# Optimization experiments

Measured on AMD Instinct MI355X. Metric: run time of the kernel, lower is better.

## Reference

```python
import jax, jax.numpy as jnp
import numpy as np

HIDDEN = 128
N_RBF = 20
K = 16
CUTOFF = 5.0


def setup_inputs() -> dict:
    key = jax.random.key(0)
    ks = jax.random.split(key, 12)
    B, N, D = 8, 4096, HIDDEN
    edge_in = 2 * D + N_RBF  # 276
    s = 0.02
    return {
        "h": jax.random.normal(ks[0], (B, N, D), jnp.float32),
        "positions": jax.random.normal(ks[1], (B, N, 3), jnp.float32),
        # edge MLP: Linear(276->128), SiLU, Linear(128->128), SiLU
        "ew1": jax.random.normal(ks[2], (edge_in, D), jnp.float32) * s,
        "eb1": jnp.zeros((D,), jnp.float32),
        "ew2": jax.random.normal(ks[3], (D, D), jnp.float32) * s,
        "eb2": jnp.zeros((D,), jnp.float32),
        # node MLP: Linear(256->128), SiLU, (Dropout=identity in eval), Linear(128->128)
        "nw1": jax.random.normal(ks[4], (2 * D, D), jnp.float32) * s,
        "nb1": jnp.zeros((D,), jnp.float32),
        "nw2": jax.random.normal(ks[5], (D, D), jnp.float32) * s,
        "nb2": jnp.zeros((D,), jnp.float32),
        # LayerNorm
        "gamma": jnp.ones((D,), jnp.float32),
        "beta": jnp.zeros((D,), jnp.float32),
    }


def reference(h, positions, ew1, eb1, ew2, eb2, nw1, nb1, nw2, nb2, gamma, beta):
    B, N, D = h.shape
    k = min(K, N - 1)

    # ---- kNN graph build (dense pairwise, self masked with +inf) ----
    diff = positions[:, :, None, :] - positions[:, None, :, :]      # [B,N,N,3]
    dists = jnp.sqrt(jnp.sum(diff * diff, axis=-1) + 1e-8)          # [B,N,N]
    eye = jnp.eye(N, dtype=bool)
    dists_masked = jnp.where(eye[None], jnp.inf, dists)
    _, edge_idx = jax.lax.top_k(-dists_masked, k)                   # [B,N,k] smallest dists
    edge_dist = jnp.take_along_axis(dists_masked, edge_idx, axis=-1)  # [B,N,k]
    edge_mask = edge_dist < CUTOFF                                  # [B,N,k]

    # ---- RBF distance encoding (non-trainable buffers) ----
    centers = jnp.linspace(0.0, CUTOFF, N_RBF)                      # [n_rbf]
    widths = (CUTOFF / N_RBF) ** (-2)
    rbf = jnp.exp(-widths * (edge_dist[..., None] - centers) ** 2)  # [B,N,k,n_rbf]

    # ---- gather neighbor features ----
    h_j = jax.vmap(lambda hb, ib: hb[ib])(h, edge_idx)              # [B,N,k,D]
    h_i = jnp.broadcast_to(h[:, :, None, :], h_j.shape)             # [B,N,k,D]
    edge_features = jnp.concatenate([h_i, h_j, rbf], axis=-1)       # [B,N,k,2D+n_rbf]

    # ---- edge MLP + mask + scatter-sum aggregate ----
    m = jax.nn.silu(edge_features @ ew1 + eb1)
    m = jax.nn.silu(m @ ew2 + eb2)
    m = m * edge_mask[..., None].astype(m.dtype)
    agg = jnp.sum(m, axis=2)                                        # [B,N,D]

    # ---- node MLP (dropout is identity at eval) + residual + LayerNorm ----
    node_in = jnp.concatenate([h, agg], axis=-1)                    # [B,N,2D]
    update = jax.nn.silu(node_in @ nw1 + nb1) @ nw2 + nb2
    x = h + update
    mu = jnp.mean(x, axis=-1, keepdims=True)
    var = jnp.mean((x - mu) ** 2, axis=-1, keepdims=True)
    return (x - mu) / jnp.sqrt(var + 1e-5) * gamma + beta
```

## Files before the change

### kernel.cpp

```cpp
#include <hip/hip_runtime.h>

#define HID 128
#define NRBF 20
#define KNN 16
#define NNODE 4096
#define NBATCH 8
#define CAP 112

typedef __attribute__((ext_vector_type(8))) short short8;
typedef __attribute__((ext_vector_type(4))) float f32x4;

__device__ __forceinline__ short f2bf(float x) {
  unsigned u = __builtin_bit_cast(unsigned, x);
  u = u + 0x7FFFu + ((u >> 16) & 1u);
  return (short)(u >> 16);
}
__device__ __forceinline__ float silu_f(float x) {
  return x * __builtin_amdgcn_rcpf(1.0f + __expf(-x));
}
__device__ __forceinline__ short8 cv8(const float* p) {
  f32x4 a = *(const f32x4*)p;
  f32x4 b = *(const f32x4*)(p + 4);
  short8 r;
  r[0]=f2bf(a[0]); r[1]=f2bf(a[1]); r[2]=f2bf(a[2]); r[3]=f2bf(a[3]);
  r[4]=f2bf(b[0]); r[5]=f2bf(b[1]); r[6]=f2bf(b[2]); r[7]=f2bf(b[3]);
  return r;
}

__global__ __launch_bounds__(256)
void hcvt_kernel(const float* __restrict__ h, short* __restrict__ hb)
{
  size_t i = ((size_t)blockIdx.x * 256 + threadIdx.x) * 8;
  *(short8*)(hb + i) = cv8(h + i);
}

__global__ __launch_bounds__(512)
void knn_kernel(const float* __restrict__ pos,
                int* __restrict__ eidx, float* __restrict__ edist)
{
  __shared__ float pX[NNODE], pY[NNODE], pZ[NNODE];
  __shared__ float d2b[8][4][CAP];
  __shared__ int   jb[8][4][CAP];
  __shared__ int   cntL[8][4];

  const int tid  = threadIdx.x;
  const int wv   = tid >> 6;
  const int lane = tid & 63;
  const int b    = blockIdx.x >> 7;
  const int grp  = blockIdx.x & 127;

  const float* pb = pos + (size_t)b * NNODE * 3;
  for (int idx = tid; idx < NNODE; idx += 512) {
    pX[idx] = pb[idx*3]; pY[idx] = pb[idx*3+1]; pZ[idx] = pb[idx*3+2];
  }
  __syncthreads();

  const int i0 = grp * 32 + wv * 4;
  float pix[4], piy[4], piz[4];
  #pragma unroll
  for (int n = 0; n < 4; ++n) { pix[n]=pX[i0+n]; piy[n]=pY[i0+n]; piz[n]=pZ[i0+n]; }

  float vmin0[4] = {3.0e38f, 3.0e38f, 3.0e38f, 3.0e38f};
  float vmin1[4] = {3.0e38f, 3.0e38f, 3.0e38f, 3.0e38f};
  #pragma unroll 4
  for (int t = 0; t < 64; t += 2) {
    const int j0 = t*64 + lane, j1 = j0 + 64;
    const float x0 = pX[j0], y0 = pY[j0], z0 = pZ[j0];
    const float x1 = pX[j1], y1 = pY[j1], z1 = pZ[j1];
    #pragma unroll
    for (int n = 0; n < 4; ++n) {
      float dx0 = pix[n]-x0, dy0 = piy[n]-y0, dz0 = piz[n]-z0;
      vmin0[n] = fminf(vmin0[n], fmaf(dz0,dz0, fmaf(dy0,dy0, dx0*dx0)));
      float dx1 = pix[n]-x1, dy1 = piy[n]-y1, dz1 = piz[n]-z1;
      vmin1[n] = fminf(vmin1[n], fmaf(dz1,dz1, fmaf(dy1,dy1, dx1*dx1)));
    }
  }

  float Tp[4];
  #pragma unroll
  for (int n = 0; n < 4; ++n) {
    float v = fminf(vmin0[n], vmin1[n]);
    #pragma unroll
    for (int k = 2; k <= 64; k <<= 1) {
      #pragma unroll
      for (int jj = k >> 1; jj > 0; jj >>= 1) {
        float o = __shfl_xor(v, jj);
        const bool up   = ((lane & k) == 0);
        const bool lowl = ((lane & jj) == 0);
        float mn = fminf(v, o), mx = fmaxf(v, o);
        v = (up == lowl) ? mn : mx;
      }
    }
    float Tf = __shfl(v, 16);
    Tp[n] = Tf * (1.0f + 2.0e-6f) + 1.0e-35f;
  }

  if (lane < 4) cntL[wv][lane] = 0;
  #pragma unroll 2
  for (int t = 0; t < 64; ++t) {
    const int j = t * 64 + lane;
    const float x = pX[j], y = pY[j], z = pZ[j];
    #pragma unroll
    for (int n = 0; n < 4; ++n) {
      float dx = pix[n] - x, dy = piy[n] - y, dz = piz[n] - z;
      float d2 = fmaf(dz, dz, fmaf(dy, dy, dx * dx));
      if ((j != i0 + n) && (d2 <= Tp[n])) {
        int p = atomicAdd(&cntL[wv][n], 1);
        if (p < CAP) jb[wv][n][p] = j;
      }
    }
  }

  #pragma unroll 1
  for (int n = 0; n < 4; ++n) {
    int cnt = cntL[wv][n];
    if (cnt > CAP) cnt = CAP;
    for (int s = lane; s < cnt; s += 64) {
      int j = jb[wv][n][s];
      float dx = __fsub_rn(pix[n], pX[j]);
      float dy = __fsub_rn(piy[n], pY[j]);
      float dz = __fsub_rn(piz[n], pZ[j]);
      d2b[wv][n][s] = __fadd_rn(__fadd_rn(__fmul_rn(dx,dx), __fmul_rn(dy,dy)),
                                __fmul_rn(dz,dz));
    }
    for (int s = lane; s < cnt; s += 64) {
      float dm = d2b[wv][n][s]; int jm = jb[wv][n][s];
      int rank = 0;
      for (int c = 0; c < cnt; ++c) {
        float dc = d2b[wv][n][c]; int jc = jb[wv][n][c];
        if (dc < dm || (dc == dm && jc < jm)) ++rank;
      }
      if (rank < KNN) {
        size_t base = ((size_t)b * NNODE + i0 + n) * KNN;
        eidx[base + rank]  = b * NNODE + jm;
        edist[base + rank] = sqrtf(__fadd_rn(dm, 1e-8f));
      }
    }
  }
}

#define ENPW 16

template<bool HBF>
__global__ __launch_bounds__(512)
void edge_kernel(const float* __restrict__ h, const short* __restrict__ hb,
                 const int* __restrict__ eidx, const float* __restrict__ edist,
                 const float* __restrict__ ew1, const float* __restrict__ eb1,
                 const float* __restrict__ ew2, const float* __restrict__ eb2,
                 float* __restrict__ agg)
{
  __shared__ __attribute__((aligned(16))) short8 F1[9*8*64];
  __shared__ __attribute__((aligned(16))) short8 F2[4*8*64];
  __shared__ __attribute__((aligned(16))) short m1s[8][2048];

  const int tid = threadIdx.x;
  for (int f = tid; f < 9*8*64; f += 512) {
    int kc = f >> 9, rem = f & 511, nf = rem >> 6, ln = rem & 63;
    int kb = kc*32 + (ln >> 4)*8, col = nf*16 + (ln & 15);
    short8 v;
    #pragma unroll
    for (int e = 0; e < 8; ++e) {
      int k = kb + e;
      v[e] = (k < 276) ? f2bf(ew1[k*128 + col]) : (short)0;
    }
    F1[f] = v;
  }
  for (int f = tid; f < 4*8*64; f += 512) {
    int kc = f >> 9, rem = f & 511, nf = rem >> 6, ln = rem & 63;
    int kb = kc*32 + (ln >> 4)*8, col = nf*16 + (ln & 15);
    short8 v;
    #pragma unroll
    for (int e = 0; e < 8; ++e) v[e] = f2bf(ew2[(kb + e)*128 + col]);
    F2[f] = v;
  }
  __syncthreads();

  const int wv = tid >> 6, lane = tid & 63;
  const int lo = lane & 15, hi = lane >> 4;
  short* m1w = &m1s[wv][0];

  float b1v[8], b2v[8];
  #pragma unroll
  for (int nf = 0; nf < 8; ++nf) {
    b1v[nf] = eb1[nf*16 + lo];
    b2v[nf] = eb2[nf*16 + lo];
  }
  int wbase[4], xmask[4], rbase[4];
  #pragma unroll
  for (int q = 0; q < 4; ++q) {
    int row = hi*4 + q;
    wbase[q] = (row << 8) + (lo << 1);
    xmask[q] = (row & 7) << 4;
  }
  #pragma unroll
  for (int kc = 0; kc < 4; ++kc)
    rbase[kc] = ((lo << 8) + ((kc*32 + hi*8) << 1)) ^ ((lo & 7) << 4);

  const f32x4 zero4 = {0.f, 0.f, 0.f, 0.f};
  const int nbase = (blockIdx.x * 8 + wv) * ENPW;

  int   jgA_p = eidx[(size_t)(nbase+0)*KNN + lo] & (NBATCH*NNODE - 1);
  int   jgB_p = eidx[(size_t)(nbase+1)*KNN + lo] & (NBATCH*NNODE - 1);
  float deA_p = edist[(size_t)(nbase+0)*KNN + lo];
  float deB_p = edist[(size_t)(nbase+1)*KNN + lo];

  #pragma unroll 1
  for (int it = 0; it < ENPW/2; ++it) {
    const int nA = nbase + it*2, nB = nA + 1;
    const int jgA = jgA_p, jgB = jgB_p;
    const float deA = deA_p, deB = deB_p;

    short8 aIA[4], aJA[4], aIB[4], aJB[4];
    #pragma unroll
    for (int kc = 0; kc < 4; ++kc) {
      if constexpr (HBF) {
        aIA[kc] = *(const short8*)(hb + (size_t)nA*HID  + kc*32 + hi*8);
        aJA[kc] = *(const short8*)(hb + (size_t)jgA*HID + kc*32 + hi*8);
        aIB[kc] = *(const short8*)(hb + (size_t)nB*HID  + kc*32 + hi*8);
        aJB[kc] = *(const short8*)(hb + (size_t)jgB*HID + kc*32 + hi*8);
      } else {
        aIA[kc] = cv8(h + (size_t)nA*HID  + kc*32 + hi*8);
        aJA[kc] = cv8(h + (size_t)jgA*HID + kc*32 + hi*8);
        aIB[kc] = cv8(h + (size_t)nB*HID  + kc*32 + hi*8);
        aJB[kc] = cv8(h + (size_t)jgB*HID + kc*32 + hi*8);
      }
    }

    if (it < ENPW/2 - 1) {
      jgA_p = eidx[(size_t)(nA+2)*KNN + lo] & (NBATCH*NNODE - 1);
      jgB_p = eidx[(size_t)(nB+2)*KNN + lo] & (NBATCH*NNODE - 1);
      deA_p = edist[(size_t)(nA+2)*KNN + lo];
      deB_p = edist[(size_t)(nB+2)*KNN + lo];
    }

    short8 aRA, aRB;
    #pragma unroll
    for (int e = 0; e < 8; ++e) {
      const int r = hi*8 + e;
      float vA = 0.f, vB = 0.f;
      if (r < NRBF) {
        const float cr = (float)(r * (5.0/19.0));
        float tA = __fsub_rn(deA, cr), tB = __fsub_rn(deB, cr);
        vA = __expf(-16.0f * __fmul_rn(tA, tA));
        vB = __expf(-16.0f * __fmul_rn(tB, tB));
      }
      aRA[e] = f2bf(vA); aRB[e] = f2bf(vB);
    }

    f32x4 acc1A[8], acc1B[8];
    #pragma unroll
    for (int nf = 0; nf < 8; ++nf) { acc1A[nf] = zero4; acc1B[nf] = zero4; }
    __builtin_amdgcn_s_setprio(1);
    #pragma unroll
    for (int kc = 0; kc < 9; ++kc) {
      short8 aA = (kc < 4) ? aIA[kc] : ((kc < 8) ? aJA[kc-4] : aRA);
      short8 aB = (kc < 4) ? aIB[kc] : ((kc < 8) ? aJB[kc-4] : aRB);
      #pragma unroll
      for (int nf = 0; nf < 8; ++nf) {
        short8 bfv = F1[(kc*8 + nf)*64 + lane];
        acc1A[nf] = __builtin_amdgcn_mfma_f32_16x16x32_bf16(aA, bfv, acc1A[nf], 0,0,0);
        acc1B[nf] = __builtin_amdgcn_mfma_f32_16x16x32_bf16(aB, bfv, acc1B[nf], 0,0,0);
      }
    }
    __builtin_amdgcn_s_setprio(0);

    short8 a2A[4], a2B[4];
    #pragma unroll
    for (int nf = 0; nf < 8; ++nf) {
      #pragma unroll
      for (int q = 0; q < 4; ++q) {
        int off = (wbase[q] + (nf << 5)) ^ xmask[q];
        *(short*)((char*)m1w + off) = f2bf(silu_f(acc1A[nf][q] + b1v[nf]));
      }
    }
    #pragma unroll
    for (int kc = 0; kc < 4; ++kc)
      a2A[kc] = *(const short8*)((char*)m1w + rbase[kc]);
    #pragma unroll
    for (int nf = 0; nf < 8; ++nf) {
      #pragma unroll
      for (int q = 0; q < 4; ++q) {
        int off = (wbase[q] + (nf << 5)) ^ xmask[q];
        *(short*)((char*)m1w + off) = f2bf(silu_f(acc1B[nf][q] + b1v[nf]));
      }
    }
    #pragma unroll
    for (int kc = 0; kc < 4; ++kc)
      a2B[kc] = *(const short8*)((char*)m1w + rbase[kc]);

    f32x4 acc2A[8], acc2B[8];
    #pragma unroll
    for (int nf = 0; nf < 8; ++nf) { acc2A[nf] = zero4; acc2B[nf] = zero4; }
    __builtin_amdgcn_s_setprio(1);
    #pragma unroll
    for (int kc = 0; kc < 4; ++kc) {
      #pragma unroll
      for (int nf = 0; nf < 8; ++nf) {
        short8 bfv = F2[(kc*8 + nf)*64 + lane];
        acc2A[nf] = __builtin_amdgcn_mfma_f32_16x16x32_bf16(a2A[kc], bfv, acc2A[nf], 0,0,0);
        acc2B[nf] = __builtin_amdgcn_mfma_f32_16x16x32_bf16(a2B[kc], bfv, acc2B[nf], 0,0,0);
      }
    }
    __builtin_amdgcn_s_setprio(0);

    float dqA[4], dqB[4];
    #pragma unroll
    for (int q = 0; q < 4; ++q) {
      dqA[q] = __shfl(deA, hi*4 + q);
      dqB[q] = __shfl(deB, hi*4 + q);
    }
    #pragma unroll
    for (int nf = 0; nf < 8; ++nf) {
      float sA = 0.f, sB = 0.f;
      #pragma unroll
      for (int q = 0; q < 4; ++q) {
        float mA = silu_f(acc2A[nf][q] + b2v[nf]);
        float mB = silu_f(acc2B[nf][q] + b2v[nf]);
        sA += (dqA[q] < 5.0f) ? mA : 0.f;
        sB += (dqB[q] < 5.0f) ? mB : 0.f;
      }
      sA += __shfl_xor(sA, 16); sA += __shfl_xor(sA, 32);
      sB += __shfl_xor(sB, 16); sB += __shfl_xor(sB, 32);
      if (hi == 0) {
        agg[(size_t)nA*HID + nf*16 + lo] = sA;
        agg[(size_t)nB*HID + nf*16 + lo] = sB;
      }
    }
  }
}

template<bool HBF>
__global__ __launch_bounds__(512)
void node_kernel(const float* __restrict__ h, const short* __restrict__ hb,
                 const float* agg,
                 const float* __restrict__ nw1, const float* __restrict__ nb1,
                 const float* __restrict__ nw2, const float* __restrict__ nb2,
                 const float* __restrict__ gam, const float* __restrict__ bet,
                 float* out)
{
  __shared__ __attribute__((aligned(16))) short8 G1[8*8*64];
  __shared__ __attribute__((aligned(16))) short8 G2[4*8*64];
  __shared__ __attribute__((aligned(16))) short m1s[8][2048];

  const int tid = threadIdx.x;
  for (int f = tid; f < 8*8*64; f += 512) {
    int kc = f >> 9, rem = f & 511, nf = rem >> 6, ln = rem & 63;
    int kb = kc*32 + (ln >> 4)*8, col = nf*16 + (ln & 15);
    short8 v;
    #pragma unroll
    for (int e = 0; e < 8; ++e) v[e] = f2bf(nw1[(kb + e)*128 + col]);
    G1[f] = v;
  }
  for (int f = tid; f < 4*8*64; f += 512) {
    int kc = f >> 9, rem = f & 511, nf = rem >> 6, ln = rem & 63;
    int kb = kc*32 + (ln >> 4)*8, col = nf*16 + (ln & 15);
    short8 v;
    #pragma unroll
    for (int e = 0; e < 8; ++e) v[e] = f2bf(nw2[(kb + e)*128 + col]);
    G2[f] = v;
  }
  __syncthreads();

  const int wv = tid >> 6, lane = tid & 63;
  const int lo = lane & 15, hi = lane >> 4;
  short* m1w = &m1s[wv][0];

  float b1v[8], b2v[8], gv[8], bv[8];
  #pragma unroll
  for (int nf = 0; nf < 8; ++nf) {
    b1v[nf] = nb1[nf*16 + lo];
    b2v[nf] = nb2[nf*16 + lo];
    gv[nf]  = gam[nf*16 + lo];
    bv[nf]  = bet[nf*16 + lo];
  }
  const f32x4 zero4 = {0.f, 0.f, 0.f, 0.f};

  const int row0 = (blockIdx.x * 8 + wv) * 16;

  const float* hrow = h   + (size_t)(row0 + lo) * HID;
  const float* arow = agg + (size_t)(row0 + lo) * HID;
  const short* hbrow = hb + (size_t)(row0 + lo) * HID;

  f32x4 acc1[8];
  #pragma unroll
  for (int nf = 0; nf < 8; ++nf) acc1[nf] = zero4;
  #pragma unroll
  for (int kc = 0; kc < 8; ++kc) {
    short8 a;
    if (kc < 4) {
      if constexpr (HBF) a = *(const short8*)(hbrow + kc*32 + hi*8);
      else               a = cv8(hrow + kc*32 + hi*8);
    } else {
      a = cv8(arow + (kc - 4)*32 + hi*8);
    }
    #pragma unroll
    for (int nf = 0; nf < 8; ++nf) {
      short8 bfv = G1[(kc*8 + nf)*64 + lane];
      acc1[nf] = __builtin_amdgcn_mfma_f32_16x16x32_bf16(a, bfv, acc1[nf], 0,0,0);
    }
  }

  #pragma unroll
  for (int nf = 0; nf < 8; ++nf) {
    #pragma unroll
    for (int q = 0; q < 4; ++q) {
      float s = silu_f(acc1[nf][q] + b1v[nf]);
      int row = hi*4 + q, col = nf*16 + lo;
      int byteoff = ((row << 8) + (col << 1)) ^ ((row & 7) << 4);
      *(short*)((char*)m1w + byteoff) = f2bf(s);
    }
  }

  f32x4 acc2[8];
  #pragma unroll
  for (int nf = 0; nf < 8; ++nf) acc2[nf] = zero4;
  #pragma unroll
  for (int kc = 0; kc < 4; ++kc) {
    int byteA = ((lo << 8) + ((kc*32 + hi*8) << 1)) ^ ((lo & 7) << 4);
    short8 a = *(const short8*)((char*)m1w + byteA);
    #pragma unroll
    for (int nf = 0; nf < 8; ++nf) {
      short8 bfv = G2[(kc*8 + nf)*64 + lane];
      acc2[nf] = __builtin_amdgcn_mfma_f32_16x16x32_bf16(a, bfv, acc2[nf], 0,0,0);
    }
  }

  float xv[4][8];
  #pragma unroll
  for (int nf = 0; nf < 8; ++nf) {
    #pragma unroll
    for (int q = 0; q < 4; ++q) {
      xv[q][nf] = acc2[nf][q] + b2v[nf]
                + h[(size_t)(row0 + hi*4 + q) * HID + nf*16 + lo];
    }
  }

  #pragma unroll
  for (int q = 0; q < 4; ++q) {
    float s = 0.0f;
    #pragma unroll
    for (int nf = 0; nf < 8; ++nf) s += xv[q][nf];
    s += __shfl_xor(s, 1); s += __shfl_xor(s, 2);
    s += __shfl_xor(s, 4); s += __shfl_xor(s, 8);
    float mu = s * 0.0078125f;
    float t = 0.0f;
    #pragma unroll
    for (int nf = 0; nf < 8; ++nf) { float d = xv[q][nf] - mu; t += d * d; }
    t += __shfl_xor(t, 1); t += __shfl_xor(t, 2);
    t += __shfl_xor(t, 4); t += __shfl_xor(t, 8);
    float inv = 1.0f / sqrtf(t * 0.0078125f + 1e-5f);
    #pragma unroll
    for (int nf = 0; nf < 8; ++nf) {
      float y = (xv[q][nf] - mu) * inv * gv[nf] + bv[nf];
      out[(size_t)(row0 + hi*4 + q) * HID + nf*16 + lo] = y;
    }
  }
}

extern "C" void kernel_launch(void* const* d_in, const int* in_sizes, int n_in,
                              void* d_out, int out_size, void* d_ws, size_t ws_size,
                              hipStream_t stream) {
  (void)in_sizes; (void)n_in; (void)out_size;
  const float* h   = (const float*)d_in[0];
  const float* pos = (const float*)d_in[1];
  const float* ew1 = (const float*)d_in[2];
  const float* eb1 = (const float*)d_in[3];
  const float* ew2 = (const float*)d_in[4];
  const float* eb2 = (const float*)d_in[5];
  const float* nw1 = (const float*)d_in[6];
  const float* nb1 = (const float*)d_in[7];
  const float* nw2 = (const float*)d_in[8];
  const float* nb2 = (const float*)d_in[9];
  const float* gam = (const float*)d_in[10];
  const float* bet = (const float*)d_in[11];

  const size_t base_need = (size_t)NBATCH * NNODE * KNN * 8;
  const size_t hbf_need  = base_need + (size_t)NBATCH * NNODE * HID * 2;
  if (ws_size < base_need) return;
  const bool use_hbf = (ws_size >= hbf_need);

  char* wsp = (char*)d_ws;
  int*   eidx  = (int*)wsp;
  float* edist = (float*)(wsp + (size_t)NBATCH * NNODE * KNN * 4);
  short* hb    = (short*)(wsp + base_need);
  float* agg   = (float*)d_out;

  if (use_hbf) {
    hcvt_kernel<<<dim3(2048), dim3(256), 0, stream>>>(h, hb);
  }
  knn_kernel<<<dim3(1024), dim3(512), 0, stream>>>(pos, eidx, edist);
  if (use_hbf) {
    edge_kernel<true ><<<dim3(256), dim3(512), 0, stream>>>(h, hb, eidx, edist,
                                                            ew1, eb1, ew2, eb2, agg);
    node_kernel<true ><<<dim3(256), dim3(512), 0, stream>>>(h, hb, agg, nw1, nb1,
                                                            nw2, nb2, gam, bet, (float*)d_out);
  } else {
    edge_kernel<false><<<dim3(256), dim3(512), 0, stream>>>(h, hb, eidx, edist,
                                                            ew1, eb1, ew2, eb2, agg);
    node_kernel<false><<<dim3(256), dim3(512), 0, stream>>>(h, hb, agg, nw1, nb1,
                                                            nw2, nb2, gam, bet, (float*)d_out);
  }
}
```

Baseline: 207.1 us.

## Pre-pack edge MLP weights once and stream W1 fragments from global

```diff
diff --git a/kernel.cpp b/kernel.cpp
--- a/kernel.cpp
+++ b/kernel.cpp
@@ -25,6 +25,32 @@
   r[0]=f2bf(a[0]); r[1]=f2bf(a[1]); r[2]=f2bf(a[2]); r[3]=f2bf(a[3]);
   r[4]=f2bf(b[0]); r[5]=f2bf(b[1]); r[6]=f2bf(b[2]); r[7]=f2bf(b[3]);
   return r;
+}
+
+__global__ __launch_bounds__(256)
+void wprep_kernel(const float* __restrict__ ew1, const float* __restrict__ ew2,
+                  short8* __restrict__ wb1, short8* __restrict__ wb2)
+{
+  int f = blockIdx.x * 256 + threadIdx.x;
+  if (f < 9*8*64) {
+    int kc = f >> 9, rem = f & 511, nf = rem >> 6, ln = rem & 63;
+    int kb = kc*32 + (ln >> 4)*8, col = nf*16 + (ln & 15);
+    short8 v;
+    #pragma unroll
+    for (int e = 0; e < 8; ++e) {
+      int k = kb + e;
+      v[e] = (k < 276) ? f2bf(ew1[k*128 + col]) : (short)0;
+    }
+    wb1[f] = v;
+  } else if (f < 9*8*64 + 4*8*64) {
+    int g = f - 9*8*64;
+    int kc = g >> 9, rem = g & 511, nf = rem >> 6, ln = rem & 63;
+    int kb = kc*32 + (ln >> 4)*8, col = nf*16 + (ln & 15);
+    short8 v;
+    #pragma unroll
+    for (int e = 0; e < 8; ++e) v[e] = f2bf(ew2[(kb + e)*128 + col]);
+    wb2[g] = v;
+  }
 }
 
 __global__ __launch_bounds__(256)
@@ -139,40 +165,21 @@
   }
 }
 
-#define ENPW 16
+#define ENPW 8
 
 template<bool HBF>
 __global__ __launch_bounds__(512)
 void edge_kernel(const float* __restrict__ h, const short* __restrict__ hb,
                  const int* __restrict__ eidx, const float* __restrict__ edist,
-                 const float* __restrict__ ew1, const float* __restrict__ eb1,
-                 const float* __restrict__ ew2, const float* __restrict__ eb2,
+                 const short8* __restrict__ wb1, const short8* __restrict__ wb2,
+                 const float* __restrict__ eb1, const float* __restrict__ eb2,
                  float* __restrict__ agg)
 {
-  __shared__ __attribute__((aligned(16))) short8 F1[9*8*64];
   __shared__ __attribute__((aligned(16))) short8 F2[4*8*64];
   __shared__ __attribute__((aligned(16))) short m1s[8][2048];
 
   const int tid = threadIdx.x;
-  for (int f = tid; f < 9*8*64; f += 512) {
-    int kc = f >> 9, rem = f & 511, nf = rem >> 6, ln = rem & 63;
-    int kb = kc*32 + (ln >> 4)*8, col = nf*16 + (ln & 15);
-    short8 v;
-    #pragma unroll
-    for (int e = 0; e < 8; ++e) {
-      int k = kb + e;
-      v[e] = (k < 276) ? f2bf(ew1[k*128 + col]) : (short)0;
-    }
-    F1[f] = v;
-  }
-  for (int f = tid; f < 4*8*64; f += 512) {
-    int kc = f >> 9, rem = f & 511, nf = rem >> 6, ln = rem & 63;
-    int kb = kc*32 + (ln >> 4)*8, col = nf*16 + (ln & 15);
-    short8 v;
-    #pragma unroll
-    for (int e = 0; e < 8; ++e) v[e] = f2bf(ew2[(kb + e)*128 + col]);
-    F2[f] = v;
-  }
+  for (int f = tid; f < 4*8*64; f += 512) F2[f] = wb2[f];
   __syncthreads();
 
   const int wv = tid >> 6, lane = tid & 63;
@@ -199,16 +206,13 @@
   const f32x4 zero4 = {0.f, 0.f, 0.f, 0.f};
   const int nbase = (blockIdx.x * 8 + wv) * ENPW;
 
-  int   jgA_p = eidx[(size_t)(nbase+0)*KNN + lo] & (NBATCH*NNODE - 1);
-  int   jgB_p = eidx[(size_t)(nbase+1)*KNN + lo] & (NBATCH*NNODE - 1);
-  float deA_p = edist[(size_t)(nbase+0)*KNN + lo];
-  float deB_p = edist[(size_t)(nbase+1)*KNN + lo];
-
   #pragma unroll 1
   for (int it = 0; it < ENPW/2; ++it) {
     const int nA = nbase + it*2, nB = nA + 1;
-    const int jgA = jgA_p, jgB = jgB_p;
-    const float deA = deA_p, deB = deB_p;
+    int jgA = eidx[(size_t)nA*KNN + lo] & (NBATCH*NNODE - 1);
+    int jgB = eidx[(size_t)nB*KNN + lo] & (NBATCH*NNODE - 1);
+    const float deA = edist[(size_t)nA*KNN + lo];
+    const float deB = edist[(size_t)nB*KNN + lo];
 
     short8 aIA[4], aJA[4], aIB[4], aJB[4];
     #pragma unroll
@@ -225,14 +229,6 @@
         aJB[kc] = cv8(h + (size_t)jgB*HID + kc*32 + hi*8);
       }
     }
-
-    if (it < ENPW/2 - 1) {
-      jgA_p = eidx[(size_t)(nA+2)*KNN + lo] & (NBATCH*NNODE - 1);
-      jgB_p = eidx[(size_t)(nB+2)*KNN + lo] & (NBATCH*NNODE - 1);
-      deA_p = edist[(size_t)(nA+2)*KNN + lo];
-      deB_p = edist[(size_t)(nB+2)*KNN + lo];
-    }
-
     short8 aRA, aRB;
     #pragma unroll
     for (int e = 0; e < 8; ++e) {
@@ -257,7 +253,7 @@
       short8 aB = (kc < 4) ? aIB[kc] : ((kc < 8) ? aJB[kc-4] : aRB);
       #pragma unroll
       for (int nf = 0; nf < 8; ++nf) {
-        short8 bfv = F1[(kc*8 + nf)*64 + lane];
+        short8 bfv = wb1[(kc*8 + nf)*64 + lane];
         acc1A[nf] = __builtin_amdgcn_mfma_f32_16x16x32_bf16(aA, bfv, acc1A[nf], 0,0,0);
         acc1B[nf] = __builtin_amdgcn_mfma_f32_16x16x32_bf16(aB, bfv, acc1B[nf], 0,0,0);
       }
@@ -474,29 +470,35 @@
   const float* gam = (const float*)d_in[10];
   const float* bet = (const float*)d_in[11];
 
-  const size_t base_need = (size_t)NBATCH * NNODE * KNN * 8;
-  const size_t hbf_need  = base_need + (size_t)NBATCH * NNODE * HID * 2;
-  if (ws_size < base_need) return;
-  const bool use_hbf = (ws_size >= hbf_need);
+  const size_t sz_ed  = (size_t)NBATCH * NNODE * KNN * 8;
+  const size_t sz_wb1 = (size_t)(9*8*64) * 16;
+  const size_t sz_wb2 = (size_t)(4*8*64) * 16;
+  const size_t sz_hb  = (size_t)NBATCH * NNODE * HID * 2;
+  const size_t need   = sz_ed + sz_wb1 + sz_wb2;
+  if (ws_size < need) return;
+  const bool use_hbf = (ws_size >= need + sz_hb);
 
   char* wsp = (char*)d_ws;
-  int*   eidx  = (int*)wsp;
-  float* edist = (float*)(wsp + (size_t)NBATCH * NNODE * KNN * 4);
-  short* hb    = (short*)(wsp + base_need);
-  float* agg   = (float*)d_out;
-
+  int*    eidx  = (int*)wsp;
+  float*  edist = (float*)(wsp + sz_ed / 2);
+  short8* wb1   = (short8*)(wsp + sz_ed);
+  short8* wb2   = (short8*)(wsp + sz_ed + sz_wb1);
+  short*  hb    = (short*)(wsp + need);
+  float*  agg   = (float*)d_out;
+
+  wprep_kernel<<<dim3(26), dim3(256), 0, stream>>>(ew1, ew2, wb1, wb2);
   if (use_hbf) {
     hcvt_kernel<<<dim3(2048), dim3(256), 0, stream>>>(h, hb);
   }
   knn_kernel<<<dim3(1024), dim3(512), 0, stream>>>(pos, eidx, edist);
   if (use_hbf) {
-    edge_kernel<true ><<<dim3(256), dim3(512), 0, stream>>>(h, hb, eidx, edist,
-                                                            ew1, eb1, ew2, eb2, agg);
+    edge_kernel<true ><<<dim3(512), dim3(512), 0, stream>>>(h, hb, eidx, edist,
+                                                            wb1, wb2, eb1, eb2, agg);
     node_kernel<true ><<<dim3(256), dim3(512), 0, stream>>>(h, hb, agg, nw1, nb1,
                                                             nw2, nb2, gam, bet, (float*)d_out);
   } else {
-    edge_kernel<false><<<dim3(256), dim3(512), 0, stream>>>(h, hb, eidx, edist,
-                                                            ew1, eb1, ew2, eb2, agg);
+    edge_kernel<false><<<dim3(512), dim3(512), 0, stream>>>(h, hb, eidx, edist,
+                                                            wb1, wb2, eb1, eb2, agg);
     node_kernel<false><<<dim3(256), dim3(512), 0, stream>>>(h, hb, agg, nw1, nb1,
                                                             nw2, nb2, gam, bet, (float*)d_out);
   }
```

After: 381.2 us. 84.1% more time.
